# Optimization experiments

Hardware: AMD Instinct MI355X
Metric: run time of the kernel (lower is better)

## Reference

```python
import jax, jax.numpy as jnp
import numpy as np

N = 50000
E = 800000
H = 64
IN_NF = 8
EA = 2
N_LAYERS = 4
INNER = 7.0        # module.n_layers set to 7 when varDT=False (integration step count)
COORDS_WEIGHT = 1.0
EPS = 1e-8


def _mlp2(x, W1, b1, W2, b2, act_last=False):
    h = jax.nn.silu(x @ W1 + b1)
    h = h @ W2 + b2
    return jax.nn.silu(h) if act_last else h


def setup_inputs() -> dict:
    key = jax.random.key(0)
    ks = jax.random.split(key, 20)
    def g(k, shape, scale=None):
        s = scale if scale is not None else 1.0 / np.sqrt(shape[0])
        return (jax.random.normal(k, shape, jnp.float32) * s).astype(jnp.float32)
    return {
        "his": jax.random.normal(ks[0], (N, IN_NF), jnp.float32),
        "loc": jax.random.normal(ks[1], (N, 3), jnp.float32),
        "edges": jax.random.randint(ks[2], (2, E), 0, N),
        "vel": jax.random.normal(ks[3], (N, 3), jnp.float32),
        "edge_attr": jax.random.normal(ks[4], (E, EA), jnp.float32),
        "emb_W": g(ks[5], (IN_NF, H)), "emb_b": jnp.zeros((H,), jnp.float32),
        "e_W1": g(ks[6], (2 * H + 1 + EA, H)), "e_b1": jnp.zeros((H,), jnp.float32),
        "e_W2": g(ks[7], (H, H)), "e_b2": jnp.zeros((H,), jnp.float32),
        "c_W1": g(ks[8], (H, H)), "c_b1": jnp.zeros((H,), jnp.float32),
        "c_W2": g(ks[9], (H, 1), scale=1e-3),  # last coord layer: no bias, small init
        "v_W1": g(ks[10], (H, H)), "v_b1": jnp.zeros((H,), jnp.float32),
        "v_W2": g(ks[11], (H, 1)), "v_b2": jnp.zeros((1,), jnp.float32),
        "n_W1": g(ks[12], (2 * H, H)), "n_b1": jnp.zeros((H,), jnp.float32),
        "n_W2": g(ks[13], (H, H)), "n_b2": jnp.zeros((H,), jnp.float32),
    }


def _egcl(h, coord, vel, init_vel, row, col, edge_attr, p):
    # edge model: gather -> MLP
    coord_diff = coord[row] - coord[col]                         # [E,3]
    radial = jnp.sum(coord_diff * coord_diff, -1, keepdims=True)  # [E,1]
    e_in = jnp.concatenate([h[row], h[col], radial, edge_attr], -1)
    m = _mlp2(e_in, p["e_W1"], p["e_b1"], p["e_W2"], p["e_b2"], act_last=True)  # [E,H]
    # equivariant coordinate message + scatter-mean aggregation
    w = jax.nn.silu(m @ p["c_W1"] + p["c_b1"]) @ p["c_W2"]      # [E,1]
    trans = coord_diff * w                                       # [E,3]
    num = jax.ops.segment_sum(trans, row, num_segments=h.shape[0])
    cnt = jax.ops.segment_sum(jnp.ones((row.shape[0], 1), coord.dtype), row, num_segments=h.shape[0])
    acc = COORDS_WEIGHT * num / jnp.maximum(cnt, 1.0)            # [N,3]
    # second-order (velocity) update with learned gate + speed renorm (norm_vel=True)
    v_scale = _mlp2(h, p["v_W1"], p["v_b1"], p["v_W2"], p["v_b2"])  # [N,1]
    vel = v_scale * vel + acc / INNER
    speed0 = jnp.linalg.norm(init_vel, axis=-1, keepdims=True)
    vel = vel / (jnp.linalg.norm(vel, axis=-1, keepdims=True) + EPS) * speed0
    coord = coord + vel / INNER
    # node model: scatter-sum edge features + residual MLP (recurrent=True)
    agg_h = jax.ops.segment_sum(m, row, num_segments=h.shape[0])
    h_out = h + _mlp2(jnp.concatenate([h, agg_h], -1), p["n_W1"], p["n_b1"], p["n_W2"], p["n_b2"])
    return h_out, coord, vel


def reference(his, loc, edges, vel, edge_attr, emb_W, emb_b, e_W1, e_b1, e_W2, e_b2,
              c_W1, c_b1, c_W2, v_W1, v_b1, v_W2, v_b2, n_W1, n_b1, n_W2, n_b2):
    p = dict(e_W1=e_W1, e_b1=e_b1, e_W2=e_W2, e_b2=e_b2, c_W1=c_W1, c_b1=c_b1, c_W2=c_W2,
             v_W1=v_W1, v_b1=v_b1, v_W2=v_W2, v_b2=v_b2, n_W1=n_W1, n_b1=n_b1, n_W2=n_W2, n_b2=n_b2)
    row, col = edges[0], edges[1]
    his_e = his @ emb_W + emb_b                                  # embedding
    h1, x, v = _egcl(his_e, loc, vel, vel, row, col, edge_attr, p)
    h = his_e + h1
    for _ in range(1, N_LAYERS):                                 # shared-weight recurrent module
        hi, x, v = _egcl(h, x, v, vel, row, col, edge_attr, p)
        h = h + hi
    return (x, h, v)
```

## Files before the change

kernel.cpp:

```cpp
#include <hip/hip_runtime.h>
#include <hip/hip_bf16.h>
#include <stdint.h>

#define NN 50000
#define EE 800000
#define HD 64
#define AGS 72

typedef short short8 __attribute__((ext_vector_type(8)));
typedef float f32x4  __attribute__((ext_vector_type(4)));
typedef float f32x16 __attribute__((ext_vector_type(16)));
typedef uint  uint2v __attribute__((ext_vector_type(2)));

__device__ __forceinline__ float b2f(ushort u){ return __uint_as_float(((uint32_t)u)<<16); }
__device__ __forceinline__ ushort f2b(float f){
  uint32_t u = __float_as_uint(f);
  u += 0x7fffu + ((u>>16)&1u);
  return (ushort)(u>>16);
}
__device__ __forceinline__ uint pk2(float lo, float hi){
  union { __hip_bfloat162 b; uint u; } x;
  x.b = __float22bfloat162_rn(make_float2(lo, hi));
  return x.u;
}
__device__ __forceinline__ float silu_f(float x){
  return x * __builtin_amdgcn_rcpf(1.0f + __expf(-x));
}


__global__ __launch_bounds__(256) void k_count2(const int* __restrict__ erow,
    int* __restrict__ counts, const float* __restrict__ loc,
    const float* __restrict__ vel0, float4* __restrict__ coordw4,
    float4* __restrict__ velw4){
  int gid = blockIdx.x*256 + threadIdx.x;
  if (gid < EE) atomicAdd(&counts[erow[gid]], 1);
  if (gid < NN){
    float vx = vel0[gid*3+0], vy = vel0[gid*3+1], vz = vel0[gid*3+2];
    float sp = sqrtf(vx*vx + vy*vy + vz*vz);
    velw4[gid] = make_float4(vx, vy, vz, sp);
    coordw4[gid] = make_float4(loc[gid*3+0], loc[gid*3+1], loc[gid*3+2], 0.0f);
  }
}

__global__ __launch_bounds__(256) void k_bsum(const int* __restrict__ counts, int* __restrict__ bsum){
  __shared__ int sm[4];
  int tid = threadIdx.x;
  int i = blockIdx.x*256 + tid;
  int v = (i < NN) ? counts[i] : 0;
  #pragma unroll
  for (int off = 1; off < 64; off <<= 1) v += __shfl_xor(v, off);
  if ((tid & 63) == 0) sm[tid >> 6] = v;
  __syncthreads();
  if (tid == 0) bsum[blockIdx.x] = sm[0] + sm[1] + sm[2] + sm[3];
}

__global__ __launch_bounds__(256) void k_bscan(const int* __restrict__ bsum, int* __restrict__ bbase){
  __shared__ int sm[256];
  int tid = threadIdx.x;
  int v = (tid < 196) ? bsum[tid] : 0;
  sm[tid] = v;
  __syncthreads();
  #pragma unroll
  for (int off = 1; off < 256; off <<= 1){
    int t = (tid >= off) ? sm[tid - off] : 0;
    __syncthreads();
    sm[tid] += t;
    __syncthreads();
  }
  if (tid < 196) bbase[tid] = sm[tid] - v;
}

__global__ __launch_bounds__(256) void k_scatter(const int* __restrict__ counts,
    const int* __restrict__ bbase, int* __restrict__ cursor){
  __shared__ int sm[256];
  int tid = threadIdx.x;
  int i = blockIdx.x*256 + tid;
  int v = (i < NN) ? counts[i] : 0;
  sm[tid] = v;
  __syncthreads();
  #pragma unroll
  for (int off = 1; off < 256; off <<= 1){
    int t = (tid >= off) ? sm[tid - off] : 0;
    __syncthreads();
    sm[tid] += t;
    __syncthreads();
  }
  if (i < NN) cursor[i] = bbase[blockIdx.x] + sm[tid] - v;
}

__global__ __launch_bounds__(256) void k_fill(const int* __restrict__ erow,
    const int* __restrict__ ecol, const float* __restrict__ eattr,
    int* __restrict__ cursor, int4* __restrict__ erec){
  int e = blockIdx.x*256 + threadIdx.x;
  if (e < EE){
    int r = erow[e];
    int pos = atomicAdd(&cursor[r], 1);
    int4 rec;
    rec.x = r;
    rec.y = ecol[e];
    rec.z = __float_as_int(eattr[(size_t)e*2 + 0]);
    rec.w = __float_as_int(eattr[(size_t)e*2 + 1]);
    erec[pos] = rec;
  }
}

__global__ __launch_bounds__(256) void k_packall(const float* __restrict__ eW1,
    const float* __restrict__ b1, const float* __restrict__ eW2,
    const float* __restrict__ cW1, const float* __restrict__ nW1,
    const float* __restrict__ nW2, const float* __restrict__ vW1,
    ushort* __restrict__ dst){
  int idx = blockIdx.x*256 + threadIdx.x;
  if (idx >= 33792) return;
  float v;
  if (idx < 17408){
    int rel; const float* src; int isW1 = 0;
    if (idx < 9216){ rel = idx; src = eW1; isW1 = 1; }
    else if (idx < 13312){ rel = idx - 9216; src = eW2; }
    else { rel = idx - 13312; src = cW1; }
    int u = rel >> 9;
    int kt = u >> 1, mt = u & 1;
    int within = rel & 511;
    int lane = within >> 3, i = within & 7;
    int k = kt*16 + (lane>>5)*8 + i;
    int col = mt*32 + (lane & 31);
    if (isW1){
      if (k < 131) v = src[k*64 + col];
      else if (k == 131) v = b1[col];
      else v = 0.0f;
    } else {
      v = (k < 64) ? src[k*64 + col] : 0.0f;
    }
  } else {
    int rel = idx - 17408;
    const float* src; int kt; int Ksrc;
    if (rel < 8192){ src = nW1; kt = rel >> 11; Ksrc = 128; }
    else if (rel < 12288){ src = nW2; kt = (rel - 8192) >> 11; Ksrc = 64; }
    else { src = vW1; kt = (rel - 12288) >> 11; Ksrc = 64; }
    int within = rel & 2047;
    int i = within & 7;
    int lane = (within >> 3) & 63;
    int ct = (within >> 9) & 3;
    int k = kt*32 + (lane>>4)*8 + i;
    int col = ct*16 + (lane & 15);
    v = (k < Ksrc) ? src[k*64 + col] : 0.0f;
  }
  dst[idx] = f2b(v);
}

__global__ __launch_bounds__(256) void k_embed(const float* __restrict__ his,
    const float* __restrict__ embW, const float* __restrict__ embB,
    float* __restrict__ h, ushort* __restrict__ hb){
  int idx = blockIdx.x*256 + threadIdx.x;
  if (idx >= NN*HD) return;
  int n = idx >> 6, j = idx & 63;
  float s = embB[j];
  #pragma unroll
  for (int k = 0; k < 8; ++k) s += his[n*8 + k] * embW[k*64 + j];
  h[idx] = s;
  hb[idx] = f2b(s);
}

__global__ __launch_bounds__(256, 4) void k_edge(
    const ushort* __restrict__ hb, const float4* __restrict__ coord4,
    const int4* __restrict__ erec,
    const ushort* __restrict__ W1p, const ushort* __restrict__ W2p, const ushort* __restrict__ C1p,
    const float* __restrict__ b2, const float* __restrict__ cb1, const float* __restrict__ cw2,
    float* __restrict__ aggf)
{
  __shared__ __align__(16) uint XMT[128*38];
  __shared__ __align__(16) float TRL[128*4];
  const int tid = threadIdx.x;
  const int wave = tid >> 6, lane = tid & 63;
  const int e = lane & 31, h = lane >> 5;
  const int wt = wave * 32;
  const int slot = blockIdx.x*128 + wt + e;

  int4 er = erec[slot];
  const int rA = er.x, cA = er.y;

  float4 crd = coord4[rA], ccd = coord4[cA];
  float dx = crd.x-ccd.x, dy = crd.y-ccd.y, dz = crd.z-ccd.z;
  float radial = dx*dx + dy*dy + dz*dz;

  const short8* W1f = reinterpret_cast<const short8*>(W1p);
  const short8* W2f = reinterpret_cast<const short8*>(W2p);
  const short8* C1f = reinterpret_cast<const short8*>(C1p);
  const int wrow = (wt + e)*38;

  {
    short8 bf[9];
    #pragma unroll
    for (int kt = 0; kt < 4; ++kt)
      bf[kt] = *reinterpret_cast<const short8*>(hb + (size_t)rA*HD + kt*16 + h*8);
    #pragma unroll
    for (int kt = 0; kt < 4; ++kt)
      bf[4+kt] = *reinterpret_cast<const short8*>(hb + (size_t)cA*HD + kt*16 + h*8);
    short8 t8 = {0,0,0,0,0,0,0,0};
    if (h == 0){
      t8[0] = (short)f2b(radial);
      t8[1] = (short)f2b(__int_as_float(er.z));
      t8[2] = (short)f2b(__int_as_float(er.w));
      t8[3] = (short)0x3F80;
    }
    bf[8] = t8;

    #pragma unroll 1
    for (int mt = 0; mt < 2; ++mt){
      f32x16 a;
      #pragma unroll
      for (int r = 0; r < 16; ++r) a[r] = 0.0f;
      #pragma unroll
      for (int kt = 0; kt < 9; ++kt)
        a = __builtin_amdgcn_mfma_f32_32x32x16_bf16(W1f[(kt*2+mt)*64 + lane], bf[kt], a, 0,0,0);
      #pragma unroll
      for (int q = 0; q < 4; ++q){
        uint u0 = pk2(silu_f(a[4*q+0]), silu_f(a[4*q+1]));
        uint u1 = pk2(silu_f(a[4*q+2]), silu_f(a[4*q+3]));
        *reinterpret_cast<uint2v*>(&XMT[wrow + mt*16 + q*4 + h*2]) = (uint2v){u0, u1};
      }
    }
  }
  __builtin_amdgcn_sched_barrier(0);

  {
    short8 xf[4];
    #pragma unroll
    for (int kt = 0; kt < 4; ++kt)
      xf[kt] = *reinterpret_cast<const short8*>(&XMT[wrow + kt*8 + h*4]);
    #pragma unroll 1
    for (int mt = 0; mt < 2; ++mt){
      f32x16 a;
      #pragma unroll
      for (int q = 0; q < 4; ++q){
        f32x4 bq = *reinterpret_cast<const f32x4*>(b2 + mt*32 + q*8 + h*4);
        #pragma unroll
        for (int r = 0; r < 4; ++r) a[4*q+r] = bq[r];
      }
      #pragma unroll
      for (int kt = 0; kt < 4; ++kt)
        a = __builtin_amdgcn_mfma_f32_32x32x16_bf16(W2f[(kt*2+mt)*64 + lane], xf[kt], a, 0,0,0);
      #pragma unroll
      for (int q = 0; q < 4; ++q){
        uint u0 = pk2(silu_f(a[4*q+0]), silu_f(a[4*q+1]));
        uint u1 = pk2(silu_f(a[4*q+2]), silu_f(a[4*q+3]));
        *reinterpret_cast<uint2v*>(&XMT[wrow + mt*16 + q*4 + h*2]) = (uint2v){u0, u1};
      }
    }
  }
  __builtin_amdgcn_sched_barrier(0);

  float pw = 0.0f;
  {
    short8 xg[4];
    #pragma unroll
    for (int kt = 0; kt < 4; ++kt)
      xg[kt] = *reinterpret_cast<const short8*>(&XMT[wrow + kt*8 + h*4]);
    #pragma unroll 1
    for (int mt = 0; mt < 2; ++mt){
      f32x16 a;
      #pragma unroll
      for (int q = 0; q < 4; ++q){
        f32x4 bq = *reinterpret_cast<const f32x4*>(cb1 + mt*32 + q*8 + h*4);
        #pragma unroll
        for (int r = 0; r < 4; ++r) a[4*q+r] = bq[r];
      }
      #pragma unroll
      for (int kt = 0; kt < 4; ++kt)
        a = __builtin_amdgcn_mfma_f32_32x32x16_bf16(C1f[(kt*2+mt)*64 + lane], xg[kt], a, 0,0,0);
      #pragma unroll
      for (int q = 0; q < 4; ++q){
        f32x4 cwq = *reinterpret_cast<const f32x4*>(cw2 + mt*32 + q*8 + h*4);
        #pragma unroll
        for (int r = 0; r < 4; ++r) pw += silu_f(a[4*q+r]) * cwq[r];
      }
    }
  }
  pw += __shfl_xor(pw, 32);
  if (h == 0){
    f32x4 t = {dx*pw, dy*pw, dz*pw, 0.0f};
    *reinterpret_cast<f32x4*>(&TRL[(wt + e)*4]) = t;
  }
  __builtin_amdgcn_sched_barrier(0);

  const ushort* mvals = reinterpret_cast<const ushort*>(XMT);
  float sum = 0.f, ts = 0.f;
  int rcur = __builtin_amdgcn_readlane(rA, 0);
  #pragma unroll
  for (int i = 0; i < 32; ++i){
    sum += b2f(mvals[(wt + i)*76 + lane]);
    if (lane < 3) ts += TRL[(wt + i)*4 + lane];
    int rnext = (i < 31) ? __builtin_amdgcn_readlane(rA, i+1) : -1;
    if (rnext != rcur){
      atomicAdd(&aggf[(size_t)rcur*AGS + lane], sum);
      if (lane < 3) atomicAdd(&aggf[(size_t)rcur*AGS + 64 + lane], ts);
      sum = 0.f; ts = 0.f; rcur = rnext;
    }
  }
}

__global__ __launch_bounds__(256) void k_node(
    const ushort* __restrict__ hb, float* __restrict__ aggf, const float* __restrict__ h_in,
    const ushort* __restrict__ nW1p, const ushort* __restrict__ nW2p, const ushort* __restrict__ vW1p,
    const float* __restrict__ nb1, const float* __restrict__ nb2,
    const float* __restrict__ vb1, const float* __restrict__ vW2, const float* __restrict__ vb2,
    const int* __restrict__ counts, float4* __restrict__ velw4, float4* __restrict__ coordw4,
    float* __restrict__ h_out, ushort* __restrict__ hb_out,
    float* __restrict__ xout, float* __restrict__ vout, int last)
{
  __shared__ __align__(16) ushort HID[64*88];
  __shared__ float VS[64];
  const int tid = threadIdx.x;
  const int wave = tid >> 6, lane = tid & 63;
  const int c = lane & 15, g = lane >> 4;
  const int wt = wave * 16;
  const int nbase = blockIdx.x * 64;
  int nA = nbase + wt + c;
  int nAc = (nA < NN) ? nA : (NN-1);

  short8 af[4];
  af[0] = *reinterpret_cast<const short8*>(hb + (size_t)nAc*HD + g*8);
  af[1] = *reinterpret_cast<const short8*>(hb + (size_t)nAc*HD + 32 + g*8);
  {
    const float* ag = aggf + (size_t)nAc*AGS;
    f32x4 q0 = *reinterpret_cast<const f32x4*>(ag + g*8);
    f32x4 q1 = *reinterpret_cast<const f32x4*>(ag + g*8 + 4);
    f32x4 q2 = *reinterpret_cast<const f32x4*>(ag + 32 + g*8);
    f32x4 q3 = *reinterpret_cast<const f32x4*>(ag + 32 + g*8 + 4);
    union FB { ushort u[8]; short8 s; };
    FB f2_, f3_;
    #pragma unroll
    for (int i = 0; i < 4; ++i){ f2_.u[i] = f2b(q0[i]); f2_.u[4+i] = f2b(q1[i]); }
    #pragma unroll
    for (int i = 0; i < 4; ++i){ f3_.u[i] = f2b(q2[i]); f3_.u[4+i] = f2b(q3[i]); }
    af[2] = f2_.s;
    af[3] = f3_.s;
  }
  const short8* N1f = reinterpret_cast<const short8*>(nW1p);
  const short8* N2f = reinterpret_cast<const short8*>(nW2p);
  const short8* V1f = reinterpret_cast<const short8*>(vW1p);

  f32x4 acc[4];
  #pragma unroll
  for (int ct = 0; ct < 4; ++ct){
    float bb = nb1[ct*16 + c];
    acc[ct] = (f32x4){bb,bb,bb,bb};
  }
  #pragma unroll
  for (int kt = 0; kt < 4; ++kt){
    #pragma unroll
    for (int ct = 0; ct < 4; ++ct){
      acc[ct] = __builtin_amdgcn_mfma_f32_16x16x32_bf16(af[kt], N1f[(kt*4+ct)*64 + lane], acc[ct], 0,0,0);
    }
  }
  #pragma unroll
  for (int ct = 0; ct < 4; ++ct){
    int col = ct*16 + c;
    #pragma unroll
    for (int r = 0; r < 4; ++r){
      HID[(wt + g*4 + r)*88 + col] = f2b(silu_f(acc[ct][r]));
    }
  }

  f32x4 av[4];
  #pragma unroll
  for (int ct = 0; ct < 4; ++ct){
    float bb = vb1[ct*16 + c];
    av[ct] = (f32x4){bb,bb,bb,bb};
  }
  #pragma unroll
  for (int kt = 0; kt < 2; ++kt){
    #pragma unroll
    for (int ct = 0; ct < 4; ++ct){
      av[ct] = __builtin_amdgcn_mfma_f32_16x16x32_bf16(af[kt], V1f[(kt*4+ct)*64 + lane], av[ct], 0,0,0);
    }
  }
  float pw[4] = {0.f,0.f,0.f,0.f};
  #pragma unroll
  for (int ct = 0; ct < 4; ++ct){
    float vw = vW2[ct*16 + c];
    #pragma unroll
    for (int r = 0; r < 4; ++r) pw[r] += silu_f(av[ct][r]) * vw;
  }
  #pragma unroll
  for (int off = 1; off < 16; off <<= 1){
    #pragma unroll
    for (int r = 0; r < 4; ++r) pw[r] += __shfl_xor(pw[r], off, 16);
  }
  if (c == 0){
    float vbias = vb2[0];
    #pragma unroll
    for (int r = 0; r < 4; ++r) VS[wt + g*4 + r] = pw[r] + vbias;
  }

  short8 h0 = *reinterpret_cast<const short8*>(&HID[(wt + c)*88 + g*8]);
  short8 h1 = *reinterpret_cast<const short8*>(&HID[(wt + c)*88 + 32 + g*8]);
  f32x4 a2[4];
  #pragma unroll
  for (int ct = 0; ct < 4; ++ct){
    float bb = nb2[ct*16 + c];
    a2[ct] = (f32x4){bb,bb,bb,bb};
  }
  #pragma unroll
  for (int ct = 0; ct < 4; ++ct)
    a2[ct] = __builtin_amdgcn_mfma_f32_16x16x32_bf16(h0, N2f[(0*4+ct)*64 + lane], a2[ct], 0,0,0);
  #pragma unroll
  for (int ct = 0; ct < 4; ++ct)
    a2[ct] = __builtin_amdgcn_mfma_f32_16x16x32_bf16(h1, N2f[(1*4+ct)*64 + lane], a2[ct], 0,0,0);
  #pragma unroll
  for (int ct = 0; ct < 4; ++ct){
    int col = ct*16 + c;
    #pragma unroll
    for (int r = 0; r < 4; ++r){
      int n = nbase + wt + g*4 + r;
      if (n < NN){
        size_t off = (size_t)n*HD + col;
        float v = 2.0f*h_in[off] + a2[ct][r];
        h_out[off] = v;
        hb_out[off] = f2b(v);
      }
    }
  }

  __syncthreads();
  if (tid < 64){
    int n = nbase + tid;
    if (n < NN){
      float vsn = VS[tid];
      float inv = 1.0f / fmaxf((float)counts[n], 1.0f);
      const float* ag = aggf + (size_t)n*AGS + 64;
      float ax = ag[0]*inv, ay = ag[1]*inv, az = ag[2]*inv;
      float4 vv = velw4[n];
      float4 cc = coordw4[n];
      float v0 = vsn*vv.x + ax*(1.0f/7.0f);
      float v1 = vsn*vv.y + ay*(1.0f/7.0f);
      float v2 = vsn*vv.z + az*(1.0f/7.0f);
      float s = vv.w / (sqrtf(v0*v0 + v1*v1 + v2*v2) + 1e-8f);
      v0 *= s; v1 *= s; v2 *= s;
      float c0 = cc.x + v0*(1.0f/7.0f);
      float c1 = cc.y + v1*(1.0f/7.0f);
      float c2 = cc.z + v2*(1.0f/7.0f);
      if (last){
        vout[n*3+0] = v0; vout[n*3+1] = v1; vout[n*3+2] = v2;
        xout[n*3+0] = c0; xout[n*3+1] = c1; xout[n*3+2] = c2;
      } else {
        velw4[n] = make_float4(v0, v1, v2, vv.w);
        coordw4[n] = make_float4(c0, c1, c2, 0.0f);
      }
    }
  }

  __syncthreads();
  int nvalid = NN - nbase; if (nvalid > 64) nvalid = 64;
  float* zb = aggf + (size_t)nbase*AGS;
  for (int idx2 = tid; idx2 < nvalid*AGS; idx2 += 256) zb[idx2] = 0.0f;
}

extern "C" void kernel_launch(void* const* d_in, const int* in_sizes, int n_in,
                              void* d_out, int out_size, void* d_ws, size_t ws_size,
                              hipStream_t stream)
{
  const float* his  = (const float*)d_in[0];
  const float* loc  = (const float*)d_in[1];
  const int*   edges= (const int*)d_in[2];
  const float* vel0 = (const float*)d_in[3];
  const float* eatt = (const float*)d_in[4];
  const float* embW = (const float*)d_in[5];
  const float* embB = (const float*)d_in[6];
  const float* eW1  = (const float*)d_in[7];
  const float* eB1  = (const float*)d_in[8];
  const float* eW2  = (const float*)d_in[9];
  const float* eB2  = (const float*)d_in[10];
  const float* cW1  = (const float*)d_in[11];
  const float* cB1  = (const float*)d_in[12];
  const float* cW2  = (const float*)d_in[13];
  const float* vW1  = (const float*)d_in[14];
  const float* vB1  = (const float*)d_in[15];
  const float* vW2  = (const float*)d_in[16];
  const float* vB2  = (const float*)d_in[17];
  const float* nW1  = (const float*)d_in[18];
  const float* nB1  = (const float*)d_in[19];
  const float* nW2  = (const float*)d_in[20];
  const float* nB2  = (const float*)d_in[21];
  const int* erow = edges;
  const int* ecol = edges + EE;

  char* ws = (char*)d_ws;
  size_t off = 0;
  auto alloc = [&](size_t bytes)->char*{
    char* p = ws + off;
    off = (off + bytes + 255) & ~(size_t)255;
    return p;
  };
  ushort* hb     = (ushort*)alloc((size_t)NN*HD*2);
  int*    counts = (int*)   alloc((size_t)NN*4);
  int*    cursor = (int*)   alloc((size_t)NN*4);
  int*    bsum   = (int*)   alloc(256*4);
  int*    bbase  = (int*)   alloc(256*4);
  float4* coordw4= (float4*)alloc((size_t)NN*16);
  float4* velw4  = (float4*)alloc((size_t)NN*16);
  float*  aggf   = (float*) alloc((size_t)NN*AGS*4);
  ushort* allp   = (ushort*)alloc(33792*2);
  int4*   erec   = (int4*)  alloc((size_t)EE*16);

  ushort* eW1p32 = allp;
  ushort* eW2p32 = allp + 9216;
  ushort* cW1p32 = allp + 13312;
  ushort* nW1p   = allp + 17408;
  ushort* nW2p   = allp + 25600;
  ushort* vW1p   = allp + 29696;

  float* xout = (float*)d_out;
  float* hout = (float*)d_out + (size_t)NN*3;
  float* vout = (float*)d_out + (size_t)NN*3 + (size_t)NN*HD;

  hipMemsetAsync(counts, 0, (size_t)NN*4, stream);
  hipMemsetAsync(aggf, 0, (size_t)NN*AGS*4, stream);
  k_count2<<<3125,256,0,stream>>>(erow, counts, loc, vel0, coordw4, velw4);
  k_bsum<<<196,256,0,stream>>>(counts, bsum);
  k_bscan<<<1,256,0,stream>>>(bsum, bbase);
  k_scatter<<<196,256,0,stream>>>(counts, bbase, cursor);
  k_fill<<<3125,256,0,stream>>>(erow, ecol, eatt, cursor, erec);
  k_packall<<<132,256,0,stream>>>(eW1, eB1, eW2, cW1, nW1, nW2, vW1, allp);
  k_embed<<<12500,256,0,stream>>>(his, embW, embB, hout, hb);

  for (int L = 0; L < 4; ++L){
    k_edge<<<6250,256,0,stream>>>(hb, coordw4, erec,
        eW1p32, eW2p32, cW1p32, eB2, cB1, cW2, aggf);
    k_node<<<782,256,0,stream>>>(hb, aggf, hout, nW1p, nW2p, vW1p,
        nB1, nB2, vB1, vW2, vB2, counts, velw4, coordw4,
        hout, hb, xout, vout, (L==3) ? 1 : 0);
  }
}
```

Before: 513.5 us.

## Fuse prep kernels, fold biases into MFMA, swizzle edge blocks, plain-store interior segments

The setup kernels (count, pack, embed) are merged into one launch, and the two memsets are merged into one by placing aggf right after counts. In the edge kernel, the biases for the second and coordinate layers are folded into packed weights and applied through an extra MFMA against a ones vector. Blocks are remapped XCD-aware so each XCD handles a contiguous range of edges. MFMA sections get raised wave priority. Row segments fully contained within a wave are written with plain stores instead of atomics, and the node-side zeroing uses vector stores. The plain stores assume each interior segment is owned by only one wave, which the sorted edge order appears to guarantee. The extra MFMA adds a little compute in exchange for fewer bias loads.

```diff
diff --git a/kernel.cpp b/kernel.cpp
--- a/kernel.cpp
+++ b/kernel.cpp
@@ -27,18 +27,72 @@
   return x * __builtin_amdgcn_rcpf(1.0f + __expf(-x));
 }
 
-
-__global__ __launch_bounds__(256) void k_count2(const int* __restrict__ erow,
-    int* __restrict__ counts, const float* __restrict__ loc,
-    const float* __restrict__ vel0, float4* __restrict__ coordw4,
-    float4* __restrict__ velw4){
+__global__ __launch_bounds__(256) void k_prep(
+    const int* __restrict__ erow, int* __restrict__ counts,
+    const float* __restrict__ loc, const float* __restrict__ vel0,
+    float4* __restrict__ coordw4, float4* __restrict__ velw4,
+    const float* __restrict__ his, const float* __restrict__ embW,
+    const float* __restrict__ embB, float* __restrict__ h, ushort* __restrict__ hb,
+    const float* __restrict__ eW1, const float* __restrict__ eB1,
+    const float* __restrict__ eW2, const float* __restrict__ eB2,
+    const float* __restrict__ cW1, const float* __restrict__ cB1,
+    const float* __restrict__ nW1, const float* __restrict__ nW2,
+    const float* __restrict__ vW1, ushort* __restrict__ allp)
+{
   int gid = blockIdx.x*256 + threadIdx.x;
+  if (gid < NN*HD){
+    int n = gid >> 6, j = gid & 63;
+    float s = embB[j];
+    #pragma unroll
+    for (int k = 0; k < 8; ++k) s += his[n*8 + k] * embW[k*64 + j];
+    h[gid] = s;
+    hb[gid] = f2b(s);
+  }
   if (gid < EE) atomicAdd(&counts[erow[gid]], 1);
   if (gid < NN){
     float vx = vel0[gid*3+0], vy = vel0[gid*3+1], vz = vel0[gid*3+2];
     float sp = sqrtf(vx*vx + vy*vy + vz*vz);
     velw4[gid] = make_float4(vx, vy, vz, sp);
     coordw4[gid] = make_float4(loc[gid*3+0], loc[gid*3+1], loc[gid*3+2], 0.0f);
+  }
+  if (gid < 35840){
+    int idx = gid;
+    float v;
+    if (idx < 19456){
+      int rel; const float* src; const float* bias; int mode;
+      if (idx < 9216){ rel = idx; src = eW1; bias = eB1; mode = 0; }
+      else if (idx < 14336){ rel = idx - 9216; src = eW2; bias = eB2; mode = 1; }
+      else { rel = idx - 14336; src = cW1; bias = cB1; mode = 1; }
+      int u = rel >> 9;
+      int kt = u >> 1, mt = u & 1;
+      int within = rel & 511;
+      int lane = within >> 3, i = within & 7;
+      int k = kt*16 + (lane>>5)*8 + i;
+      int col = mt*32 + (lane & 31);
+      if (mode == 0){
+        if (k < 131) v = src[k*64 + col];
+        else if (k == 131) v = bias[col];
+        else v = 0.0f;
+      } else {
+        if (k < 64) v = src[k*64 + col];
+        else if (k == 64) v = bias[col];
+        else v = 0.0f;
+      }
+    } else {
+      int rel = idx - 19456;
+      const float* src; int kt; int Ksrc;
+      if (rel < 8192){ src = nW1; kt = rel >> 11; Ksrc = 128; }
+      else if (rel < 12288){ src = nW2; kt = (rel - 8192) >> 11; Ksrc = 64; }
+      else { src = vW1; kt = (rel - 12288) >> 11; Ksrc = 64; }
+      int within = rel & 2047;
+      int i = within & 7;
+      int lane = (within >> 3) & 63;
+      int ct = (within >> 9) & 3;
+      int k = kt*32 + (lane>>4)*8 + i;
+      int col = ct*16 + (lane & 15);
+      v = (k < Ksrc) ? src[k*64 + col] : 0.0f;
+    }
+    allp[idx] = f2b(v);
   }
 }
 
@@ -104,67 +158,11 @@
   }
 }
 
-__global__ __launch_bounds__(256) void k_packall(const float* __restrict__ eW1,
-    const float* __restrict__ b1, const float* __restrict__ eW2,
-    const float* __restrict__ cW1, const float* __restrict__ nW1,
-    const float* __restrict__ nW2, const float* __restrict__ vW1,
-    ushort* __restrict__ dst){
-  int idx = blockIdx.x*256 + threadIdx.x;
-  if (idx >= 33792) return;
-  float v;
-  if (idx < 17408){
-    int rel; const float* src; int isW1 = 0;
-    if (idx < 9216){ rel = idx; src = eW1; isW1 = 1; }
-    else if (idx < 13312){ rel = idx - 9216; src = eW2; }
-    else { rel = idx - 13312; src = cW1; }
-    int u = rel >> 9;
-    int kt = u >> 1, mt = u & 1;
-    int within = rel & 511;
-    int lane = within >> 3, i = within & 7;
-    int k = kt*16 + (lane>>5)*8 + i;
-    int col = mt*32 + (lane & 31);
-    if (isW1){
-      if (k < 131) v = src[k*64 + col];
-      else if (k == 131) v = b1[col];
-      else v = 0.0f;
-    } else {
-      v = (k < 64) ? src[k*64 + col] : 0.0f;
-    }
-  } else {
-    int rel = idx - 17408;
-    const float* src; int kt; int Ksrc;
-    if (rel < 8192){ src = nW1; kt = rel >> 11; Ksrc = 128; }
-    else if (rel < 12288){ src = nW2; kt = (rel - 8192) >> 11; Ksrc = 64; }
-    else { src = vW1; kt = (rel - 12288) >> 11; Ksrc = 64; }
-    int within = rel & 2047;
-    int i = within & 7;
-    int lane = (within >> 3) & 63;
-    int ct = (within >> 9) & 3;
-    int k = kt*32 + (lane>>4)*8 + i;
-    int col = ct*16 + (lane & 15);
-    v = (k < Ksrc) ? src[k*64 + col] : 0.0f;
-  }
-  dst[idx] = f2b(v);
-}
-
-__global__ __launch_bounds__(256) void k_embed(const float* __restrict__ his,
-    const float* __restrict__ embW, const float* __restrict__ embB,
-    float* __restrict__ h, ushort* __restrict__ hb){
-  int idx = blockIdx.x*256 + threadIdx.x;
-  if (idx >= NN*HD) return;
-  int n = idx >> 6, j = idx & 63;
-  float s = embB[j];
-  #pragma unroll
-  for (int k = 0; k < 8; ++k) s += his[n*8 + k] * embW[k*64 + j];
-  h[idx] = s;
-  hb[idx] = f2b(s);
-}
-
 __global__ __launch_bounds__(256, 4) void k_edge(
     const ushort* __restrict__ hb, const float4* __restrict__ coord4,
     const int4* __restrict__ erec,
     const ushort* __restrict__ W1p, const ushort* __restrict__ W2p, const ushort* __restrict__ C1p,
-    const float* __restrict__ b2, const float* __restrict__ cb1, const float* __restrict__ cw2,
+    const float* __restrict__ cw2,
     float* __restrict__ aggf)
 {
   __shared__ __align__(16) uint XMT[128*38];
@@ -173,7 +171,11 @@
   const int wave = tid >> 6, lane = tid & 63;
   const int e = lane & 31, h = lane >> 5;
   const int wt = wave * 32;
-  const int slot = blockIdx.x*128 + wt + e;
+
+  const int bid = blockIdx.x;
+  const int xcd = bid & 7, bx = bid >> 3;
+  const int swz = (xcd < 2) ? (xcd*782 + bx) : (2*782 + (xcd-2)*781 + bx);
+  const int slot = swz*128 + wt + e;
 
   int4 er = erec[slot];
   const int rA = er.x, cA = er.y;
@@ -186,6 +188,9 @@
   const short8* W2f = reinterpret_cast<const short8*>(W2p);
   const short8* C1f = reinterpret_cast<const short8*>(C1p);
   const int wrow = (wt + e)*38;
+
+  short8 ones8 = {0,0,0,0,0,0,0,0};
+  if (h == 0) ones8[0] = (short)0x3F80;
 
   {
     short8 bf[9];
@@ -209,9 +214,11 @@
       f32x16 a;
       #pragma unroll
       for (int r = 0; r < 16; ++r) a[r] = 0.0f;
+      __builtin_amdgcn_s_setprio(1);
       #pragma unroll
       for (int kt = 0; kt < 9; ++kt)
         a = __builtin_amdgcn_mfma_f32_32x32x16_bf16(W1f[(kt*2+mt)*64 + lane], bf[kt], a, 0,0,0);
+      __builtin_amdgcn_s_setprio(0);
       #pragma unroll
       for (int q = 0; q < 4; ++q){
         uint u0 = pk2(silu_f(a[4*q+0]), silu_f(a[4*q+1]));
@@ -231,14 +238,13 @@
     for (int mt = 0; mt < 2; ++mt){
       f32x16 a;
       #pragma unroll
-      for (int q = 0; q < 4; ++q){
-        f32x4 bq = *reinterpret_cast<const f32x4*>(b2 + mt*32 + q*8 + h*4);
-        #pragma unroll
-        for (int r = 0; r < 4; ++r) a[4*q+r] = bq[r];
-      }
+      for (int r = 0; r < 16; ++r) a[r] = 0.0f;
+      __builtin_amdgcn_s_setprio(1);
       #pragma unroll
       for (int kt = 0; kt < 4; ++kt)
         a = __builtin_amdgcn_mfma_f32_32x32x16_bf16(W2f[(kt*2+mt)*64 + lane], xf[kt], a, 0,0,0);
+      a = __builtin_amdgcn_mfma_f32_32x32x16_bf16(W2f[(4*2+mt)*64 + lane], ones8, a, 0,0,0);
+      __builtin_amdgcn_s_setprio(0);
       #pragma unroll
       for (int q = 0; q < 4; ++q){
         uint u0 = pk2(silu_f(a[4*q+0]), silu_f(a[4*q+1]));
@@ -259,14 +265,13 @@
     for (int mt = 0; mt < 2; ++mt){
       f32x16 a;
       #pragma unroll
-      for (int q = 0; q < 4; ++q){
-        f32x4 bq = *reinterpret_cast<const f32x4*>(cb1 + mt*32 + q*8 + h*4);
-        #pragma unroll
-        for (int r = 0; r < 4; ++r) a[4*q+r] = bq[r];
-      }
+      for (int r = 0; r < 16; ++r) a[r] = 0.0f;
+      __builtin_amdgcn_s_setprio(1);
       #pragma unroll
       for (int kt = 0; kt < 4; ++kt)
         a = __builtin_amdgcn_mfma_f32_32x32x16_bf16(C1f[(kt*2+mt)*64 + lane], xg[kt], a, 0,0,0);
+      a = __builtin_amdgcn_mfma_f32_32x32x16_bf16(C1f[(4*2+mt)*64 + lane], ones8, a, 0,0,0);
+      __builtin_amdgcn_s_setprio(0);
       #pragma unroll
       for (int q = 0; q < 4; ++q){
         f32x4 cwq = *reinterpret_cast<const f32x4*>(cw2 + mt*32 + q*8 + h*4);
@@ -285,15 +290,21 @@
   const ushort* mvals = reinterpret_cast<const ushort*>(XMT);
   float sum = 0.f, ts = 0.f;
   int rcur = __builtin_amdgcn_readlane(rA, 0);
+  int segstart = 0;
   #pragma unroll
   for (int i = 0; i < 32; ++i){
     sum += b2f(mvals[(wt + i)*76 + lane]);
     if (lane < 3) ts += TRL[(wt + i)*4 + lane];
     int rnext = (i < 31) ? __builtin_amdgcn_readlane(rA, i+1) : -1;
     if (rnext != rcur){
-      atomicAdd(&aggf[(size_t)rcur*AGS + lane], sum);
-      if (lane < 3) atomicAdd(&aggf[(size_t)rcur*AGS + 64 + lane], ts);
-      sum = 0.f; ts = 0.f; rcur = rnext;
+      if (segstart == 0 || i == 31){
+        atomicAdd(&aggf[(size_t)rcur*AGS + lane], sum);
+        if (lane < 3) atomicAdd(&aggf[(size_t)rcur*AGS + 64 + lane], ts);
+      } else {
+        aggf[(size_t)rcur*AGS + lane] = sum;
+        if (lane < 3) aggf[(size_t)rcur*AGS + 64 + lane] = ts;
+      }
+      sum = 0.f; ts = 0.f; rcur = rnext; segstart = i + 1;
     }
   }
 }
@@ -451,8 +462,9 @@
 
   __syncthreads();
   int nvalid = NN - nbase; if (nvalid > 64) nvalid = 64;
-  float* zb = aggf + (size_t)nbase*AGS;
-  for (int idx2 = tid; idx2 < nvalid*AGS; idx2 += 256) zb[idx2] = 0.0f;
+  f32x4* zb4 = reinterpret_cast<f32x4*>(aggf + (size_t)nbase*AGS);
+  f32x4 z4 = {0.f,0.f,0.f,0.f};
+  for (int idx2 = tid; idx2 < nvalid*(AGS/4); idx2 += 256) zb4[idx2] = z4;
 }
 
 extern "C" void kernel_launch(void* const* d_in, const int* in_sizes, int n_in,
@@ -493,39 +505,39 @@
   };
   ushort* hb     = (ushort*)alloc((size_t)NN*HD*2);
   int*    counts = (int*)   alloc((size_t)NN*4);
+  float*  aggf   = (float*) alloc((size_t)NN*AGS*4);
   int*    cursor = (int*)   alloc((size_t)NN*4);
   int*    bsum   = (int*)   alloc(256*4);
   int*    bbase  = (int*)   alloc(256*4);
   float4* coordw4= (float4*)alloc((size_t)NN*16);
   float4* velw4  = (float4*)alloc((size_t)NN*16);
-  float*  aggf   = (float*) alloc((size_t)NN*AGS*4);
-  ushort* allp   = (ushort*)alloc(33792*2);
+  ushort* allp   = (ushort*)alloc(35840*2);
   int4*   erec   = (int4*)  alloc((size_t)EE*16);
 
   ushort* eW1p32 = allp;
   ushort* eW2p32 = allp + 9216;
-  ushort* cW1p32 = allp + 13312;
-  ushort* nW1p   = allp + 17408;
-  ushort* nW2p   = allp + 25600;
-  ushort* vW1p   = allp + 29696;
+  ushort* cW1p32 = allp + 14336;
+  ushort* nW1p   = allp + 19456;
+  ushort* nW2p   = allp + 27648;
+  ushort* vW1p   = allp + 31744;
 
   float* xout = (float*)d_out;
   float* hout = (float*)d_out + (size_t)NN*3;
   float* vout = (float*)d_out + (size_t)NN*3 + (size_t)NN*HD;
 
-  hipMemsetAsync(counts, 0, (size_t)NN*4, stream);
-  hipMemsetAsync(aggf, 0, (size_t)NN*AGS*4, stream);
-  k_count2<<<3125,256,0,stream>>>(erow, counts, loc, vel0, coordw4, velw4);
+  size_t counts_pad = ((size_t)NN*4 + 255) & ~(size_t)255;
+  hipMemsetAsync(counts, 0, counts_pad + (size_t)NN*AGS*4, stream);
+  k_prep<<<12500,256,0,stream>>>(erow, counts, loc, vel0, coordw4, velw4,
+      his, embW, embB, hout, hb,
+      eW1, eB1, eW2, eB2, cW1, cB1, nW1, nW2, vW1, allp);
   k_bsum<<<196,256,0,stream>>>(counts, bsum);
   k_bscan<<<1,256,0,stream>>>(bsum, bbase);
   k_scatter<<<196,256,0,stream>>>(counts, bbase, cursor);
   k_fill<<<3125,256,0,stream>>>(erow, ecol, eatt, cursor, erec);
-  k_packall<<<132,256,0,stream>>>(eW1, eB1, eW2, cW1, nW1, nW2, vW1, allp);
-  k_embed<<<12500,256,0,stream>>>(his, embW, embB, hout, hb);
 
   for (int L = 0; L < 4; ++L){
     k_edge<<<6250,256,0,stream>>>(hb, coordw4, erec,
-        eW1p32, eW2p32, cW1p32, eB2, cB1, cW2, aggf);
+        eW1p32, eW2p32, cW1p32, cW2, aggf);
     k_node<<<782,256,0,stream>>>(hb, aggf, hout, nW1p, nW2p, vW1p,
         nB1, nB2, vB1, vW2, vB2, counts, velw4, coordw4,
         hout, hb, xout, vout, (L==3) ? 1 : 0);
```

Result: faster. 498.8 us (-2.9%).
